# Optimization experiments

Hardware: AMD Instinct MI355X
Metric: run time of the kernel (lower is better)

The kernel has to match this reference:

```python
import jax, jax.numpy as jnp
import numpy as np

BN_EPS = 1e-5
ELU_ALPHA = 512.0  # bug-faithful: nn.ELU(in_channels) sets alpha=in_channels


def conv3x3(x, w):
    # NCHW input, OIHW kernel, stride 1, padding 1 (SAME for k=3)
    return jax.lax.conv_general_dilated(
        x, w, window_strides=(1, 1), padding=((1, 1), (1, 1)),
        dimension_numbers=('NCHW', 'OIHW', 'NCHW'))


def conv1x1(x, w, b):
    # 1x1 conv as a channel contraction
    return jnp.einsum('oc,bchw->bohw', w[:, :, 0, 0], x) + b[None, :, None, None]


def batchnorm(x, g, b, m, v):
    scale = g / jnp.sqrt(v + BN_EPS)
    return (x - m[None, :, None, None]) * scale[None, :, None, None] + b[None, :, None, None]


def cc_module(x, wq, bq, wk, bk, wv, bv, gamma):
    B, C, H, W = x.shape
    q = conv1x1(x, wq, bq)   # [B, C/8, H, W]
    k = conv1x1(x, wk, bk)   # [B, C/8, H, W]
    v = conv1x1(x, wv, bv)   # [B, C,   H, W]
    # column (H-axis) attention scores with -inf on the self-diagonal
    eH = jnp.einsum('bchw,bcgw->bhwg', q, k)              # [B,H,W,H]
    diag = jnp.eye(H, dtype=bool)[None, :, None, :]       # mask h == g
    eH = jnp.where(diag, -jnp.inf, eH)
    # row (W-axis) attention scores
    eW = jnp.einsum('bchw,bchv->bhwv', q, k)              # [B,H,W,W]
    att = jax.nn.softmax(jnp.concatenate([eH, eW], axis=-1), axis=-1)  # [B,H,W,H+W]
    aH, aW = att[..., :H], att[..., H:]
    oH = jnp.einsum('bcgw,bhwg->bchw', v, aH)
    oW = jnp.einsum('bchv,bhwv->bchw', v, aW)
    return gamma[0] * (oH + oW) + x


def setup_inputs() -> dict:
    key = jax.random.key(0)
    ks = jax.random.split(key, 20)
    B, Cin, H, W = 8, 512, 64, 64
    Ci = Cin // 4            # 128
    Cq = Ci // 8             # 16
    n = lambda k, s, sc: jax.random.normal(k, s, dtype=jnp.float32) * sc
    inp = {
        'x': n(ks[0], (B, Cin, H, W), 1.0),
        'conva_w': n(ks[1], (Ci, Cin, 3, 3), 0.02),
        'bn1_g': jax.random.uniform(ks[2], (Ci,)) + 0.5,
        'bn1_b': n(ks[3], (Ci,), 0.1),
        'bn1_m': n(ks[4], (Ci,), 0.1),
        'bn1_v': jax.random.uniform(ks[5], (Ci,)) + 0.5,
        'wq': n(ks[6], (Cq, Ci, 1, 1), 0.05),
        'bq': n(ks[7], (Cq,), 0.02),
        'wk': n(ks[8], (Cq, Ci, 1, 1), 0.05),
        'bk': n(ks[9], (Cq,), 0.02),
        'wv': n(ks[10], (Ci, Ci, 1, 1), 0.05),
        'bv': n(ks[11], (Ci,), 0.02),
        'cc_gamma': jnp.full((1,), 0.5, dtype=jnp.float32),
        'convb_w': n(ks[12], (Ci, Ci, 3, 3), 0.05),
        'bn2_g': jax.random.uniform(ks[13], (Ci,)) + 0.5,
        'bn2_b': n(ks[14], (Ci,), 0.1),
        'bn2_m': n(ks[15], (Ci,), 0.1),
        'bn2_v': jax.random.uniform(ks[16], (Ci,)) + 0.5,
        'bott_w': n(ks[17], (Cin, Cin + Ci, 3, 3), 0.02),
        'recurrence': 2,
    }
    return inp


def reference(x, conva_w, bn1_g, bn1_b, bn1_m, bn1_v,
              wq, bq, wk, bk, wv, bv, cc_gamma,
              convb_w, bn2_g, bn2_b, bn2_m, bn2_v,
              bott_w, recurrence):
    out = batchnorm(conv3x3(x, conva_w), bn1_g, bn1_b, bn1_m, bn1_v)
    for _ in range(int(recurrence)):
        out = cc_module(out, wq, bq, wk, bk, wv, bv, cc_gamma)
    out = batchnorm(conv3x3(out, convb_w), bn2_g, bn2_b, bn2_m, bn2_v)
    out = conv3x3(jnp.concatenate([x, out], axis=1), bott_w)
    # ELU with alpha = in_channels (faithful to nn.ELU(in_channels))
    return jnp.where(out > 0, out, ELU_ALPHA * jnp.expm1(out))
```

## Files before the change

### kernel.cpp

```cpp
#include <hip/hip_runtime.h>
#include <math.h>


typedef __attribute__((ext_vector_type(8))) short short8;
typedef __attribute__((ext_vector_type(4))) float f32x4;

__device__ __forceinline__ unsigned short f2bf(float x) {
    unsigned u = __float_as_uint(x);
    unsigned r = u + 0x7FFFu + ((u >> 16) & 1u);
    return (unsigned short)(r >> 16);
}
__device__ __forceinline__ float bf2f(unsigned short h) {
    return __uint_as_float(((unsigned)h) << 16);
}

__global__ __launch_bounds__(256) void prep_bn_kernel(
        const float* g1, const float* b1, const float* m1, const float* v1,
        const float* g2, const float* b2, const float* m2, const float* v2,
        float* s1o, float* h1o, float* s2o, float* h2o) {
    int t = threadIdx.x;
    if (t < 128) {
        float s = g1[t] * __frsqrt_rn(v1[t] + 1e-5f);
        s1o[t] = s; h1o[t] = b1[t] - m1[t] * s;
    } else {
        int c = t - 128;
        float s = g2[c] * __frsqrt_rn(v2[c] + 1e-5f);
        s2o[c] = s; h2o[c] = b2[c] - m2[c] * s;
    }
}

__global__ __launch_bounds__(256) void prep_w_kernel(
        const float* __restrict__ w, unsigned short* __restrict__ WH,
        unsigned short* __restrict__ WL, int CIN, int COUT) {
    int idx = blockIdx.x * 256 + threadIdx.x;
    if (idx >= COUT * CIN) return;
    int cout = idx / CIN, ci = idx - cout * CIN;
    #pragma unroll
    for (int tap = 0; tap < 9; ++tap) {
        float v = w[(size_t)idx * 9 + tap];
        unsigned short h = f2bf(v);
        unsigned short l = f2bf(v - bf2f(h));
        size_t o = ((size_t)tap * COUT + cout) * CIN + ci;
        WH[o] = h; WL[o] = l;
    }
}

__global__ __launch_bounds__(256) void prep_qkv_kernel(
        const float* __restrict__ wq, const float* __restrict__ wk,
        const float* __restrict__ wv,
        float* __restrict__ wqk_t, float* __restrict__ wv_t) {
    int e = blockIdx.x * 256 + threadIdx.x;
    if (e < 4096) {
        int ci = e >> 5, co = e & 31;
        wqk_t[e] = (co < 16) ? wq[co * 128 + ci] : wk[(co - 16) * 128 + ci];
    } else if (e < 4096 + 16384) {
        int e2 = e - 4096;
        int ci = e2 >> 7, co = e2 & 127;
        wv_t[e2] = wv[co * 128 + ci];
    }
}

__global__ __launch_bounds__(256) void transpose_cl_kernel(
        const float* __restrict__ in, float* __restrict__ out, int NCH) {
    __shared__ float T[32][260];
    const int t = threadIdx.x;
    const int h0 = blockIdx.x * 4, b = blockIdx.y, ck = blockIdx.z;
    const float* base = in + (size_t)(b * NCH + ck) * 32 * 4096;
    const int ci = t >> 3, w0 = (t & 7) * 8;
    #pragma unroll
    for (int hh = 0; hh < 4; ++hh) {
        float4 u0 = *(const float4*)&base[(size_t)ci * 4096 + (h0 + hh) * 64 + w0];
        float4 u1 = *(const float4*)&base[(size_t)ci * 4096 + (h0 + hh) * 64 + w0 + 4];
        T[ci][hh * 65 + w0 + 0] = u0.x; T[ci][hh * 65 + w0 + 1] = u0.y;
        T[ci][hh * 65 + w0 + 2] = u0.z; T[ci][hh * 65 + w0 + 3] = u0.w;
        T[ci][hh * 65 + w0 + 4] = u1.x; T[ci][hh * 65 + w0 + 5] = u1.y;
        T[ci][hh * 65 + w0 + 6] = u1.z; T[ci][hh * 65 + w0 + 7] = u1.w;
    }
    __syncthreads();
    const int w = t & 63, hh2 = t >> 6;
    float* op = out + ((size_t)((b * NCH + ck) * 4096) + (h0 + hh2) * 64 + w) * 32;
    #pragma unroll
    for (int cg = 0; cg < 8; ++cg) {
        float4 r;
        r.x = T[cg * 4 + 0][hh2 * 65 + w];
        r.y = T[cg * 4 + 1][hh2 * 65 + w];
        r.z = T[cg * 4 + 2][hh2 * 65 + w];
        r.w = T[cg * 4 + 3][hh2 * 65 + w];
        *(float4*)&op[cg * 4] = r;
    }
}

template<int NCHUNK, int COUT, int EPI, int C1CH>
__global__ __launch_bounds__(256, 2) void conv3x3_mfma_kernel(
        const float* __restrict__ xt1, const float* __restrict__ xt2,
        const unsigned short* __restrict__ WH, const unsigned short* __restrict__ WL,
        const float* __restrict__ bns, const float* __restrict__ bnb,
        float* __restrict__ out) {
    constexpr int CINF = NCHUNK * 32;
    __shared__ unsigned short XS[2][4][66][40];
    __shared__ unsigned short WAs[2][64][104];
    const int t = threadIdx.x;
    const int lane = t & 63, wave = t >> 6;
    const int ch = wave >> 1, o = wave & 1;
    const int ln = lane & 15, lg = lane >> 4;
    const int h0 = blockIdx.x * 2, b = blockIdx.y, cb0 = blockIdx.z * 64;

    if (t < 32) {
        int r = t >> 3, s = (t >> 2) & 1, cig = t & 3;
        short8 z = {};
        *(short8*)&XS[0][r][s * 65][cig * 8] = z;
        *(short8*)&XS[1][r][s * 65][cig * 8] = z;
    }

    f32x4 acc[2][4];
    #pragma unroll
    for (int mi = 0; mi < 2; ++mi)
        #pragma unroll
        for (int q = 0; q < 4; ++q) acc[mi][q] = (f32x4){0.f, 0.f, 0.f, 0.f};

    const int xr = t >> 6, xw = t & 63;
    for (int chunk = 0; chunk < NCHUNK; ++chunk) {
        const float* src = (chunk < C1CH)
            ? xt1 + (size_t)(b * C1CH + chunk) * 4096 * 32
            : xt2 + (size_t)(b * (NCHUNK - C1CH) + (chunk - C1CH)) * 4096 * 32;
        {
            int row = h0 - 1 + xr;
            if (row >= 0 && row < 64) {
                const float* sp = src + ((size_t)row * 64 + xw) * 32;
                #pragma unroll
                for (int cg = 0; cg < 4; ++cg) {
                    float4 u0 = *(const float4*)&sp[cg * 8];
                    float4 u1 = *(const float4*)&sp[cg * 8 + 4];
                    float xv[8] = {u0.x, u0.y, u0.z, u0.w, u1.x, u1.y, u1.z, u1.w};
                    short8 hi, lo;
                    #pragma unroll
                    for (int j = 0; j < 8; ++j) {
                        unsigned short hb = f2bf(xv[j]);
                        hi[j] = (short)hb;
                        lo[j] = (short)f2bf(xv[j] - bf2f(hb));
                    }
                    *(short8*)&XS[0][xr][1 + xw][cg * 8] = hi;
                    *(short8*)&XS[1][xr][1 + xw][cg * 8] = lo;
                }
            } else {
                short8 z = {};
                #pragma unroll
                for (int cg = 0; cg < 4; ++cg) {
                    *(short8*)&XS[0][xr][1 + xw][cg * 8] = z;
                    *(short8*)&XS[1][xr][1 + xw][cg * 8] = z;
                }
            }
        }
        const int ci0 = chunk * 32;
        for (int kh = 0; kh < 3; ++kh) {
            #pragma unroll
            for (int i = 0; i < 3; ++i) {
                int e = t + i * 256;
                int cout = e / 12, r2 = e - cout * 12;
                int kw = r2 >> 2, cig = r2 & 3;
                size_t go = ((size_t)(kh * 3 + kw) * COUT + cb0 + cout) * CINF + ci0 + cig * 8;
                *(short8*)&WAs[0][cout][kw * 32 + cig * 8] = *(const short8*)&WH[go];
                *(short8*)&WAs[1][cout][kw * 32 + cig * 8] = *(const short8*)&WL[go];
            }
            __syncthreads();
            const int row = o + kh;
            #pragma unroll
            for (int kw = 0; kw < 3; ++kw) {
                short8 ah0 = *(const short8*)&WAs[0][ch * 32 + ln][kw * 32 + lg * 8];
                short8 ah1 = *(const short8*)&WAs[0][ch * 32 + 16 + ln][kw * 32 + lg * 8];
                short8 al0 = *(const short8*)&WAs[1][ch * 32 + ln][kw * 32 + lg * 8];
                short8 al1 = *(const short8*)&WAs[1][ch * 32 + 16 + ln][kw * 32 + lg * 8];
                #pragma unroll
                for (int q = 0; q < 4; ++q) {
                    short8 bh = *(const short8*)&XS[0][row][q * 16 + ln + kw][lg * 8];
                    short8 bl = *(const short8*)&XS[1][row][q * 16 + ln + kw][lg * 8];
                    acc[0][q] = __builtin_amdgcn_mfma_f32_16x16x32_bf16(ah0, bh, acc[0][q], 0, 0, 0);
                    acc[1][q] = __builtin_amdgcn_mfma_f32_16x16x32_bf16(ah1, bh, acc[1][q], 0, 0, 0);
                    acc[0][q] = __builtin_amdgcn_mfma_f32_16x16x32_bf16(ah0, bl, acc[0][q], 0, 0, 0);
                    acc[1][q] = __builtin_amdgcn_mfma_f32_16x16x32_bf16(ah1, bl, acc[1][q], 0, 0, 0);
                    acc[0][q] = __builtin_amdgcn_mfma_f32_16x16x32_bf16(al0, bh, acc[0][q], 0, 0, 0);
                    acc[1][q] = __builtin_amdgcn_mfma_f32_16x16x32_bf16(al1, bh, acc[1][q], 0, 0, 0);
                }
            }
            __syncthreads();
        }
    }
    const int hh = h0 + o;
    #pragma unroll
    for (int mi = 0; mi < 2; ++mi) {
        #pragma unroll
        for (int q = 0; q < 4; ++q) {
            #pragma unroll
            for (int reg = 0; reg < 4; ++reg) {
                int cout = cb0 + ch * 32 + mi * 16 + lg * 4 + reg;
                int wv2 = q * 16 + ln;
                float val = acc[mi][q][reg];
                if (EPI == 0) val = val * bns[cout] + bnb[cout];
                else          val = (val > 0.f) ? val : 512.0f * expm1f(val);
                out[((size_t)(b * COUT + cout) * 64 + hh) * 64 + wv2] = val;
            }
        }
    }
}

__global__ __launch_bounds__(256) void qk_kernel(
        const float* __restrict__ X, const float* __restrict__ wqk_t,
        const float* __restrict__ bq, const float* __restrict__ bk,
        float* __restrict__ q, float* __restrict__ k) {
    __shared__ float xls[128][64];
    __shared__ float wls[128][32];
    const int t = threadIdx.x;
    const int h = blockIdx.x, b = blockIdx.y;
    const float* xb = X + (size_t)b * 128 * 4096 + (size_t)h * 64;
    #pragma unroll
    for (int i = 0; i < 32; ++i) {
        int e = t + i * 256;
        xls[e >> 6][e & 63] = xb[(size_t)(e >> 6) * 4096 + (e & 63)];
    }
    #pragma unroll
    for (int i = 0; i < 16; ++i) {
        int e = t + i * 256;
        wls[e >> 5][e & 31] = wqk_t[e];
    }
    __syncthreads();
    const int w = t & 63, g = t >> 6;
    const int co0 = g * 8;
    float acc[8];
    #pragma unroll
    for (int c = 0; c < 8; ++c) acc[c] = 0.f;
    #pragma unroll 8
    for (int ci = 0; ci < 128; ++ci) {
        float xv = xls[ci][w];
        float4 wa = *(const float4*)&wls[ci][co0];
        float4 wb = *(const float4*)&wls[ci][co0 + 4];
        const float* pa = (const float*)&wa;
        const float* pb = (const float*)&wb;
        #pragma unroll
        for (int c = 0; c < 4; ++c) { acc[c] += pa[c] * xv; acc[4 + c] += pb[c] * xv; }
    }
    #pragma unroll
    for (int c = 0; c < 8; ++c) {
        int co = co0 + c;
        if (co < 16) q[((size_t)(b * 16 + co) * 64 + h) * 64 + w]      = acc[c] + bq[co];
        else         k[((size_t)(b * 16 + co - 16) * 64 + h) * 64 + w] = acc[c] + bk[co - 16];
    }
}

__global__ __launch_bounds__(256) void v_kernel(
        const float* __restrict__ X, const float* __restrict__ wv_t,
        const float* __restrict__ bv, float* __restrict__ v) {
    __shared__ float xls[16][64];
    __shared__ float wls[16][128];
    const int t = threadIdx.x;
    const int n0 = blockIdx.x * 64, b = blockIdx.y;
    const int wt = t & 15, ct = t >> 4;
    const float* xb = X + (size_t)b * 128 * 4096;
    float acc[8][4] = {};
    for (int ci0 = 0; ci0 < 128; ci0 += 16) {
        #pragma unroll
        for (int i = 0; i < 4; ++i) {
            int e = t + i * 256;
            xls[e >> 6][e & 63] = xb[(size_t)(ci0 + (e >> 6)) * 4096 + n0 + (e & 63)];
        }
        #pragma unroll
        for (int i = 0; i < 8; ++i) {
            int e = t + i * 256;
            wls[e >> 7][e & 127] = wv_t[(size_t)(ci0 + (e >> 7)) * 128 + (e & 127)];
        }
        __syncthreads();
        #pragma unroll 4
        for (int ci = 0; ci < 16; ++ci) {
            float4 xv = *(const float4*)&xls[ci][wt * 4];
            float4 wa = *(const float4*)&wls[ci][ct * 8];
            float4 wb = *(const float4*)&wls[ci][ct * 8 + 4];
            const float* px = (const float*)&xv;
            const float* pa = (const float*)&wa;
            const float* pb = (const float*)&wb;
            #pragma unroll
            for (int j = 0; j < 4; ++j)
                #pragma unroll
                for (int c = 0; c < 4; ++c) {
                    acc[c][j]     += pa[c] * px[j];
                    acc[4 + c][j] += pb[c] * px[j];
                }
        }
        __syncthreads();
    }
    #pragma unroll
    for (int c = 0; c < 8; ++c) {
        int co = ct * 8 + c;
        float bb = bv[co];
        float4 r = {acc[c][0] + bb, acc[c][1] + bb, acc[c][2] + bb, acc[c][3] + bb};
        *(float4*)&v[(size_t)(b * 128 + co) * 4096 + n0 + wt * 4] = r;
    }
}

__global__ __launch_bounds__(256) void eh_kernel(
        const float* __restrict__ q, const float* __restrict__ k,
        float* __restrict__ att) {
    __shared__ float qs[16][64];
    __shared__ float ks[16][64];
    const int t = threadIdx.x;
    const int w = blockIdx.x, b = blockIdx.y;
    #pragma unroll
    for (int i = 0; i < 4; ++i) {
        int e = t + i * 256;
        int c = e >> 6, h = e & 63;
        size_t idx = ((size_t)(b * 16 + c) * 64 + h) * 64 + w;
        qs[c][h] = q[idx];
        ks[c][h] = k[idx];
    }
    __syncthreads();
    const int g0 = (t & 15) * 4, h0 = (t >> 4) * 4;
    float acc[4][4] = {};
    #pragma unroll
    for (int c = 0; c < 16; ++c) {
        float4 qv = *(const float4*)&qs[c][h0];
        float4 kv = *(const float4*)&ks[c][g0];
        const float* pq = (const float*)&qv;
        const float* pk = (const float*)&kv;
        #pragma unroll
        for (int i = 0; i < 4; ++i)
            #pragma unroll
            for (int j = 0; j < 4; ++j) acc[i][j] += pq[i] * pk[j];
    }
    #pragma unroll
    for (int i = 0; i < 4; ++i) {
        int h = h0 + i;
        int dj = h - g0;
        if (dj >= 0 && dj < 4) acc[i][dj] = -1e30f;
        float4 r = {acc[i][0], acc[i][1], acc[i][2], acc[i][3]};
        *(float4*)&att[((size_t)(b * 64 + h) * 64 + w) * 128 + g0] = r;
    }
}

__global__ __launch_bounds__(256) void ew_kernel(
        const float* __restrict__ q, const float* __restrict__ k,
        float* __restrict__ att) {
    __shared__ float qs[16][64];
    __shared__ float ks[16][64];
    const int t = threadIdx.x;
    const int h = blockIdx.x, b = blockIdx.y;
    const float* qb2 = q + (size_t)b * 65536 + (size_t)h * 64;
    const float* kb2 = k + (size_t)b * 65536 + (size_t)h * 64;
    #pragma unroll
    for (int i = 0; i < 4; ++i) {
        int e = t + i * 256;
        int c = e >> 6, wl = e & 63;
        qs[c][wl] = qb2[(size_t)c * 4096 + wl];
        ks[c][wl] = kb2[(size_t)c * 4096 + wl];
    }
    __syncthreads();
    const int tt0 = (t & 15) * 4, w0 = (t >> 4) * 4;
    float acc[4][4] = {};
    #pragma unroll
    for (int c = 0; c < 16; ++c) {
        float4 qv = *(const float4*)&qs[c][w0];
        float4 kv = *(const float4*)&ks[c][tt0];
        const float* pq = (const float*)&qv;
        const float* pk = (const float*)&kv;
        #pragma unroll
        for (int i = 0; i < 4; ++i)
            #pragma unroll
            for (int j = 0; j < 4; ++j) acc[i][j] += pq[i] * pk[j];
    }
    #pragma unroll
    for (int i = 0; i < 4; ++i) {
        float4 r = {acc[i][0], acc[i][1], acc[i][2], acc[i][3]};
        *(float4*)&att[((size_t)(b * 64 + h) * 64 + (w0 + i)) * 128 + 64 + tt0] = r;
    }
}

__global__ __launch_bounds__(128) void softmax_kernel(float* __restrict__ att) {
    const int r = blockIdx.x, t = threadIdx.x;
    float v = att[(size_t)r * 128 + t];
    float m = v;
    #pragma unroll
    for (int off = 32; off >= 1; off >>= 1) m = fmaxf(m, __shfl_xor(m, off));
    __shared__ float s1[2], s2[2];
    const int wid = t >> 6, lane = t & 63;
    if (lane == 0) s1[wid] = m;
    __syncthreads();
    m = fmaxf(s1[0], s1[1]);
    float e = expf(v - m);
    float s = e;
    #pragma unroll
    for (int off = 32; off >= 1; off >>= 1) s += __shfl_xor(s, off);
    if (lane == 0) s2[wid] = s;
    __syncthreads();
    s = s2[0] + s2[1];
    att[(size_t)r * 128 + t] = e / s;
}

__global__ __launch_bounds__(256) void oh_kernel(
        const float* __restrict__ v, const float* __restrict__ att,
        float* __restrict__ ohb) {
    __shared__ float vs2[64][128];
    __shared__ float ah2[64][65];
    const int t = threadIdx.x;
    const int w = blockIdx.x, b = blockIdx.y;
    const float* vbp = v + (size_t)b * 524288 + w;
    #pragma unroll
    for (int i = 0; i < 32; ++i) {
        int e = t + i * 256;
        vs2[e >> 7][e & 127] = vbp[((size_t)(e & 127) * 64 + (e >> 7)) * 64];
    }
    const float* abp = att + ((size_t)b * 4096 + w) * 128;
    #pragma unroll
    for (int i = 0; i < 16; ++i) {
        int e = t + i * 256;
        ah2[e >> 6][e & 63] = abp[(size_t)(e >> 6) * 8192 + (e & 63)];
    }
    __syncthreads();
    const int h0 = (t & 15) * 4, c0 = (t >> 4) * 8;
    float acc[8][4] = {};
    for (int g = 0; g < 64; ++g) {
        float4 va  = *(const float4*)&vs2[g][c0];
        float4 vb4 = *(const float4*)&vs2[g][c0 + 4];
        const float* pa = (const float*)&va;
        const float* pb = (const float*)&vb4;
        float aj[4];
        #pragma unroll
        for (int j = 0; j < 4; ++j) aj[j] = ah2[h0 + j][g];
        #pragma unroll
        for (int j = 0; j < 4; ++j)
            #pragma unroll
            for (int i2 = 0; i2 < 4; ++i2) {
                acc[i2][j]     += pa[i2] * aj[j];
                acc[4 + i2][j] += pb[i2] * aj[j];
            }
    }
    #pragma unroll
    for (int i2 = 0; i2 < 8; ++i2)
        #pragma unroll
        for (int j = 0; j < 4; ++j)
            ohb[((size_t)(b * 128 + c0 + i2) * 64 + (h0 + j)) * 64 + w] = acc[i2][j];
}

__global__ __launch_bounds__(256) void ow_final_kernel(
        const float* __restrict__ v, const float* __restrict__ att,
        const float* __restrict__ ohb, const float* __restrict__ gamma,
        const float* __restrict__ Xin, float* __restrict__ Xout) {
    __shared__ float vs2[64][129];
    __shared__ float aws[64][65];
    const int t = threadIdx.x;
    const int h = blockIdx.x, b = blockIdx.y;
    const float* vbp = v + (size_t)b * 524288 + (size_t)h * 64;
    #pragma unroll
    for (int i = 0; i < 32; ++i) {
        int e = t + i * 256;
        vs2[e & 63][e >> 6] = vbp[(size_t)(e >> 6) * 4096 + (e & 63)];
    }
    const float* abp = att + ((size_t)(b * 64 + h) * 64) * 128 + 64;
    #pragma unroll
    for (int i = 0; i < 16; ++i) {
        int e = t + i * 256;
        aws[e >> 6][e & 63] = abp[(size_t)(e >> 6) * 128 + (e & 63)];
    }
    __syncthreads();
    const int w0 = (t & 15) * 4, c0 = (t >> 4) * 8;
    float acc[8][4] = {};
    for (int tt = 0; tt < 64; ++tt) {
        float vv[8];
        #pragma unroll
        for (int i2 = 0; i2 < 8; ++i2) vv[i2] = vs2[tt][c0 + i2];
        float aw[4];
        #pragma unroll
        for (int j = 0; j < 4; ++j) aw[j] = aws[w0 + j][tt];
        #pragma unroll
        for (int i2 = 0; i2 < 8; ++i2)
            #pragma unroll
            for (int j = 0; j < 4; ++j) acc[i2][j] += vv[i2] * aw[j];
    }
    const float gm = gamma[0];
    #pragma unroll
    for (int i2 = 0; i2 < 8; ++i2) {
        size_t base = ((size_t)(b * 128 + c0 + i2) * 64 + h) * 64 + w0;
        float4 oh4 = *(const float4*)&ohb[base];
        float4 xr  = *(const float4*)&Xin[base];
        const float* po = (const float*)&oh4;
        const float* px = (const float*)&xr;
        float4 r;
        float* pr = (float*)&r;
        #pragma unroll
        for (int j = 0; j < 4; ++j) pr[j] = gm * (acc[i2][j] + po[j]) + px[j];
        *(float4*)&Xout[base] = r;
    }
}

extern "C" void kernel_launch(void* const* d_in, const int* in_sizes, int n_in,
                              void* d_out, int out_size, void* d_ws, size_t ws_size,
                              hipStream_t stream) {
    const float* x       = (const float*)d_in[0];
    const float* conva_w = (const float*)d_in[1];
    const float* bn1_g   = (const float*)d_in[2];
    const float* bn1_b   = (const float*)d_in[3];
    const float* bn1_m   = (const float*)d_in[4];
    const float* bn1_v   = (const float*)d_in[5];
    const float* wq      = (const float*)d_in[6];
    const float* bq      = (const float*)d_in[7];
    const float* wk      = (const float*)d_in[8];
    const float* bk      = (const float*)d_in[9];
    const float* wv      = (const float*)d_in[10];
    const float* bv      = (const float*)d_in[11];
    const float* gamma   = (const float*)d_in[12];
    const float* convb_w = (const float*)d_in[13];
    const float* bn2_g   = (const float*)d_in[14];
    const float* bn2_b   = (const float*)d_in[15];
    const float* bn2_m   = (const float*)d_in[16];
    const float* bn2_v   = (const float*)d_in[17];
    const float* bott_w  = (const float*)d_in[18];

    float* ws    = (float*)d_ws;
    float* A     = ws;
    float* Bb    = A     + 4194304;
    float* vbuf  = Bb    + 4194304;
    float* attb  = vbuf  + 4194304;
    float* ohb   = attb  + 4194304;
    float* qb    = ohb   + 4194304;
    float* kb    = qb    + 524288;
    float* XT_x  = kb    + 524288;
    float* wqk_t = XT_x  + 16777216;
    float* wv_t  = wqk_t + 4096;
    float* bnsA  = wv_t  + 16384;
    float* bnbA  = bnsA  + 128;
    float* bnsB  = bnbA  + 128;
    float* bnbB  = bnsB  + 128;
    unsigned short* WHa = (unsigned short*)(bnbB + 128);
    unsigned short* WLa = WHa + 589824;
    unsigned short* WHb = WLa + 589824;
    unsigned short* WLb = WHb + 147456;
    unsigned short* WHc = WLb + 147456;
    unsigned short* WLc = WHc + 2949120;
    float* XT_cc = vbuf;
    float* XT_b  = attb;

    prep_bn_kernel<<<1, 256, 0, stream>>>(bn1_g, bn1_b, bn1_m, bn1_v,
                                          bn2_g, bn2_b, bn2_m, bn2_v,
                                          bnsA, bnbA, bnsB, bnbB);
    prep_w_kernel<<<256, 256, 0, stream>>>(conva_w, WHa, WLa, 512, 128);
    prep_w_kernel<<<64, 256, 0, stream>>>(convb_w, WHb, WLb, 128, 128);
    prep_w_kernel<<<1280, 256, 0, stream>>>(bott_w, WHc, WLc, 640, 512);
    prep_qkv_kernel<<<80, 256, 0, stream>>>(wq, wk, wv, wqk_t, wv_t);

    transpose_cl_kernel<<<dim3(16, 8, 16), 256, 0, stream>>>(x, XT_x, 16);

    conv3x3_mfma_kernel<16, 128, 0, 16><<<dim3(32, 8, 2), 256, 0, stream>>>(
        XT_x, nullptr, WHa, WLa, bnsA, bnbA, A);

    float* Xi = A;
    float* Xo = Bb;
    for (int it = 0; it < 2; ++it) {
        qk_kernel<<<dim3(64, 8), 256, 0, stream>>>(Xi, wqk_t, bq, bk, qb, kb);
        v_kernel<<<dim3(64, 8), 256, 0, stream>>>(Xi, wv_t, bv, vbuf);
        eh_kernel<<<dim3(64, 8), 256, 0, stream>>>(qb, kb, attb);
        ew_kernel<<<dim3(64, 8), 256, 0, stream>>>(qb, kb, attb);
        softmax_kernel<<<32768, 128, 0, stream>>>(attb);
        oh_kernel<<<dim3(64, 8), 256, 0, stream>>>(vbuf, attb, ohb);
        ow_final_kernel<<<dim3(64, 8), 256, 0, stream>>>(vbuf, attb, ohb, gamma, Xi, Xo);
        float* tmp = Xi; Xi = Xo; Xo = tmp;
    }

    transpose_cl_kernel<<<dim3(16, 8, 4), 256, 0, stream>>>(Xi, XT_cc, 4);
    conv3x3_mfma_kernel<4, 128, 0, 4><<<dim3(32, 8, 2), 256, 0, stream>>>(
        XT_cc, nullptr, WHb, WLb, bnsB, bnbB, Bb);

    transpose_cl_kernel<<<dim3(16, 8, 4), 256, 0, stream>>>(Bb, XT_b, 4);
    conv3x3_mfma_kernel<20, 512, 1, 16><<<dim3(32, 8, 8), 256, 0, stream>>>(
        XT_x, XT_b, WHc, WLc, nullptr, nullptr, (float*)d_out);
}
```

Baseline: 1.223 ms.

## Rewrite conv3x3 with presplit bf16 inputs, 32x32 MFMA, async LDS loads; fuse softmax

The transpose kernel now splits activations into hi/lo bf16 planes in padded, halo-aware layout, so the conv kernel no longer converts fp32 on the fly. The conv kernel is restructured to use 32x32x16 bf16 MFMA with 128-thread blocks covering 4 output rows and half the width. It loads inputs via global_load_lds directly into shared memory and streams weights from a repacked per-chunk layout straight into registers with one-tap prefetch. Separately, the ew-score and softmax kernels are fused to avoid an extra pass over the attention buffer. The changes trade a larger workspace and register pressure from 8 16-wide accumulators for less conversion and launch overhead.

```diff
diff --git a/kernel.cpp b/kernel.cpp
--- a/kernel.cpp
+++ b/kernel.cpp
@@ -2,8 +2,9 @@
 #include <math.h>
 
 
-typedef __attribute__((ext_vector_type(8))) short short8;
-typedef __attribute__((ext_vector_type(4))) float f32x4;
+typedef __attribute__((ext_vector_type(8)))  short short8;
+typedef __attribute__((ext_vector_type(4)))  float f32x4;
+typedef __attribute__((ext_vector_type(16))) float f32x16;
 
 __device__ __forceinline__ unsigned short f2bf(float x) {
     unsigned u = __float_as_uint(x);
@@ -12,6 +13,20 @@
 }
 __device__ __forceinline__ float bf2f(unsigned short h) {
     return __uint_as_float(((unsigned)h) << 16);
+}
+__device__ __forceinline__ void split2(float a, float b, unsigned& hi, unsigned& lo) {
+    unsigned h;
+    asm("v_cvt_pk_bf16_f32 %0, %1, %2" : "=v"(h) : "v"(a), "v"(b));
+    float ra = a - __uint_as_float(h << 16);
+    float rb = b - __uint_as_float(h & 0xffff0000u);
+    unsigned l;
+    asm("v_cvt_pk_bf16_f32 %0, %1, %2" : "=v"(l) : "v"(ra), "v"(rb));
+    hi = h; lo = l;
+}
+__device__ __forceinline__ void gll16(const unsigned short* g, unsigned short* l) {
+    __builtin_amdgcn_global_load_lds(
+        (const __attribute__((address_space(1))) unsigned int*)g,
+        (__attribute__((address_space(3))) unsigned int*)l, 16, 0, 0);
 }
 
 __global__ __launch_bounds__(256) void prep_bn_kernel(
@@ -29,19 +44,20 @@
     }
 }
 
-__global__ __launch_bounds__(256) void prep_w_kernel(
-        const float* __restrict__ w, unsigned short* __restrict__ WH,
-        unsigned short* __restrict__ WL, int CIN, int COUT) {
+__global__ __launch_bounds__(256) void prep_w2(
+        const float* __restrict__ w, unsigned short* __restrict__ Wp, int CIN, int COUT) {
     int idx = blockIdx.x * 256 + threadIdx.x;
     if (idx >= COUT * CIN) return;
     int cout = idx / CIN, ci = idx - cout * CIN;
+    int ck = ci >> 5, cl = ci & 31;
     #pragma unroll
     for (int tap = 0; tap < 9; ++tap) {
         float v = w[(size_t)idx * 9 + tap];
         unsigned short h = f2bf(v);
         unsigned short l = f2bf(v - bf2f(h));
-        size_t o = ((size_t)tap * COUT + cout) * CIN + ci;
-        WH[o] = h; WL[o] = l;
+        size_t rb = (((size_t)ck * 9 + tap) * 2 * COUT + cout) * 32;
+        Wp[rb + cl] = h;
+        Wp[rb + (size_t)COUT * 32 + cl] = l;
     }
 }
 
@@ -60,8 +76,8 @@
     }
 }
 
-__global__ __launch_bounds__(256) void transpose_cl_kernel(
-        const float* __restrict__ in, float* __restrict__ out, int NCH) {
+__global__ __launch_bounds__(256) void transpose_split_kernel(
+        const float* __restrict__ in, unsigned short* __restrict__ out, int NCH) {
     __shared__ float T[32][260];
     const int t = threadIdx.x;
     const int h0 = blockIdx.x * 4, b = blockIdx.y, ck = blockIdx.z;
@@ -78,126 +94,155 @@
     }
     __syncthreads();
     const int w = t & 63, hh2 = t >> 6;
-    float* op = out + ((size_t)((b * NCH + ck) * 4096) + (h0 + hh2) * 64 + w) * 32;
-    #pragma unroll
-    for (int cg = 0; cg < 8; ++cg) {
-        float4 r;
-        r.x = T[cg * 4 + 0][hh2 * 65 + w];
-        r.y = T[cg * 4 + 1][hh2 * 65 + w];
-        r.z = T[cg * 4 + 2][hh2 * 65 + w];
-        r.w = T[cg * 4 + 3][hh2 * 65 + w];
-        *(float4*)&op[cg * 4] = r;
+    const int h = h0 + hh2;
+    const size_t PL = (size_t)64 * 68 * 40;
+    unsigned short* po = out + ((size_t)(b * NCH + ck) * 2) * PL;
+    unsigned hi[16], lo[16];
+    #pragma unroll
+    for (int p = 0; p < 16; ++p) {
+        float a = T[2 * p][hh2 * 65 + w];
+        float c = T[2 * p + 1][hh2 * 65 + w];
+        split2(a, c, hi[p], lo[p]);
+    }
+    uint4 zz = {0u, 0u, 0u, 0u};
+    #pragma unroll
+    for (int half = 0; half < 2; ++half) {
+        bool ok = half ? (w >= 31) : (w <= 32);
+        int slot = half ? (w - 31) : (w + 1);
+        if (ok) {
+            unsigned short* ph = po + ((size_t)h * 68 + half * 34 + slot) * 40;
+            unsigned short* pl = ph + PL;
+            #pragma unroll
+            for (int q = 0; q < 4; ++q) {
+                uint4 hv = {hi[q * 4], hi[q * 4 + 1], hi[q * 4 + 2], hi[q * 4 + 3]};
+                uint4 lv = {lo[q * 4], lo[q * 4 + 1], lo[q * 4 + 2], lo[q * 4 + 3]};
+                *(uint4*)(ph + q * 8) = hv;
+                *(uint4*)(pl + q * 8) = lv;
+            }
+            *(uint4*)(ph + 32) = zz;
+            *(uint4*)(pl + 32) = zz;
+        }
+    }
+    if (w == 0 || w == 63) {
+        int half = (w == 63);
+        int slot = half ? 33 : 0;
+        unsigned short* ph = po + ((size_t)h * 68 + half * 34 + slot) * 40;
+        #pragma unroll
+        for (int q = 0; q < 5; ++q) {
+            *(uint4*)(ph + q * 8) = zz;
+            *(uint4*)(ph + PL + q * 8) = zz;
+        }
     }
 }
 
 template<int NCHUNK, int COUT, int EPI, int C1CH>
-__global__ __launch_bounds__(256, 2) void conv3x3_mfma_kernel(
-        const float* __restrict__ xt1, const float* __restrict__ xt2,
-        const unsigned short* __restrict__ WH, const unsigned short* __restrict__ WL,
+__global__ __launch_bounds__(128, 2) void conv3x3_g(
+        const unsigned short* __restrict__ xt1, const unsigned short* __restrict__ xt2,
+        const unsigned short* __restrict__ Wp,
         const float* __restrict__ bns, const float* __restrict__ bnb,
         float* __restrict__ out) {
-    constexpr int CINF = NCHUNK * 32;
-    __shared__ unsigned short XS[2][4][66][40];
-    __shared__ unsigned short WAs[2][64][104];
-    const int t = threadIdx.x;
-    const int lane = t & 63, wave = t >> 6;
-    const int ch = wave >> 1, o = wave & 1;
-    const int ln = lane & 15, lg = lane >> 4;
-    const int h0 = blockIdx.x * 2, b = blockIdx.y, cb0 = blockIdx.z * 64;
-
-    if (t < 32) {
-        int r = t >> 3, s = (t >> 2) & 1, cig = t & 3;
-        short8 z = {};
-        *(short8*)&XS[0][r][s * 65][cig * 8] = z;
-        *(short8*)&XS[1][r][s * 65][cig * 8] = z;
-    }
-
-    f32x4 acc[2][4];
-    #pragma unroll
-    for (int mi = 0; mi < 2; ++mi)
-        #pragma unroll
-        for (int q = 0; q < 4; ++q) acc[mi][q] = (f32x4){0.f, 0.f, 0.f, 0.f};
-
-    const int xr = t >> 6, xw = t & 63;
+    __shared__ __align__(16) unsigned short XS[2][6][34][40];
+    const int t = threadIdx.x;
+    const int lane = t & 63, ch = t >> 6;
+    const int lw = lane & 31, kg = lane >> 5;
+    const int h0 = blockIdx.x * 4;
+    const int b  = blockIdx.y;
+    const int cz = blockIdx.z >> 1, wz = blockIdx.z & 1;
+    const int cb0 = cz * 128;
+    const size_t XPLANE = (size_t)64 * 68 * 40;
+    constexpr int HLSTR = 6 * 34 * 40;
+
+    const f32x16 fz = {0.f,0.f,0.f,0.f,0.f,0.f,0.f,0.f,0.f,0.f,0.f,0.f,0.f,0.f,0.f,0.f};
+    f32x16 acc[2][4];
+    #pragma unroll
+    for (int mt = 0; mt < 2; ++mt)
+        #pragma unroll
+        for (int r = 0; r < 4; ++r) acc[mt][r] = fz;
+
+    #pragma unroll 1
     for (int chunk = 0; chunk < NCHUNK; ++chunk) {
-        const float* src = (chunk < C1CH)
-            ? xt1 + (size_t)(b * C1CH + chunk) * 4096 * 32
-            : xt2 + (size_t)(b * (NCHUNK - C1CH) + (chunk - C1CH)) * 4096 * 32;
-        {
-            int row = h0 - 1 + xr;
-            if (row >= 0 && row < 64) {
-                const float* sp = src + ((size_t)row * 64 + xw) * 32;
-                #pragma unroll
-                for (int cg = 0; cg < 4; ++cg) {
-                    float4 u0 = *(const float4*)&sp[cg * 8];
-                    float4 u1 = *(const float4*)&sp[cg * 8 + 4];
-                    float xv[8] = {u0.x, u0.y, u0.z, u0.w, u1.x, u1.y, u1.z, u1.w};
-                    short8 hi, lo;
-                    #pragma unroll
-                    for (int j = 0; j < 8; ++j) {
-                        unsigned short hb = f2bf(xv[j]);
-                        hi[j] = (short)hb;
-                        lo[j] = (short)f2bf(xv[j] - bf2f(hb));
-                    }
-                    *(short8*)&XS[0][xr][1 + xw][cg * 8] = hi;
-                    *(short8*)&XS[1][xr][1 + xw][cg * 8] = lo;
-                }
+        const unsigned short* xb = (chunk < C1CH)
+            ? xt1 + ((size_t)(b * C1CH + chunk) * 2) * XPLANE
+            : xt2 + ((size_t)(b * (NCHUNK - C1CH) + (chunk - C1CH)) * 2) * XPLANE;
+        #pragma unroll
+        for (int j = 0; j < 6; ++j) {
+            const int grow = h0 - 1 + j;
+            unsigned short* ld = &XS[ch][j][0][0];
+            if (grow >= 0 && grow < 64) {
+                const unsigned short* g = xb + (size_t)ch * XPLANE + ((size_t)grow * 68 + wz * 34) * 40;
+                gll16(g + (size_t)lane * 8, ld + (size_t)lane * 8);
+                gll16(g + (size_t)(64 + lane) * 8, ld + (size_t)(64 + lane) * 8);
+                if (lane < 42)
+                    gll16(g + (size_t)(128 + lane) * 8, ld + (size_t)(128 + lane) * 8);
             } else {
                 short8 z = {};
+                *(short8*)(ld + (size_t)lane * 8) = z;
+                *(short8*)(ld + (size_t)(64 + lane) * 8) = z;
+                if (lane < 42) *(short8*)(ld + (size_t)(128 + lane) * 8) = z;
+            }
+        }
+        __syncthreads();
+
+        const unsigned short* wbase = Wp + (size_t)chunk * (9 * 2 * (size_t)COUT * 32);
+        const int crow = cb0 + ch * 64 + lw;
+        short8 wc[8], wn[8];
+        {
+            const unsigned short* ph = wbase + ((size_t)0 * COUT + crow) * 32 + kg * 8;
+            const unsigned short* pl = ph + (size_t)COUT * 32;
+            wc[0] = *(const short8*)(ph);             wc[1] = *(const short8*)(ph + 32 * 32);
+            wc[2] = *(const short8*)(pl);             wc[3] = *(const short8*)(pl + 32 * 32);
+            wc[4] = *(const short8*)(ph + 16);        wc[5] = *(const short8*)(ph + 32 * 32 + 16);
+            wc[6] = *(const short8*)(pl + 16);        wc[7] = *(const short8*)(pl + 32 * 32 + 16);
+        }
+        #pragma unroll 1
+        for (int tap = 0; tap < 9; ++tap) {
+            {
+                const int tn = (tap < 8) ? tap + 1 : 0;
+                const unsigned short* ph = wbase + ((size_t)(tn * 2) * COUT + crow) * 32 + kg * 8;
+                const unsigned short* pl = ph + (size_t)COUT * 32;
+                wn[0] = *(const short8*)(ph);         wn[1] = *(const short8*)(ph + 32 * 32);
+                wn[2] = *(const short8*)(pl);         wn[3] = *(const short8*)(pl + 32 * 32);
+                wn[4] = *(const short8*)(ph + 16);    wn[5] = *(const short8*)(ph + 32 * 32 + 16);
+                wn[6] = *(const short8*)(pl + 16);    wn[7] = *(const short8*)(pl + 32 * 32 + 16);
+            }
+            const int kh = (tap < 3) ? 0 : ((tap < 6) ? 1 : 2);
+            const int kw = tap - kh * 3;
+            #pragma unroll
+            for (int ks = 0; ks < 2; ++ks) {
+                const short8 ah0 = wc[ks * 4 + 0], ah1 = wc[ks * 4 + 1];
+                const short8 al0 = wc[ks * 4 + 2], al1 = wc[ks * 4 + 3];
+                const int ko = ks * 16 + kg * 8;
                 #pragma unroll
-                for (int cg = 0; cg < 4; ++cg) {
-                    *(short8*)&XS[0][xr][1 + xw][cg * 8] = z;
-                    *(short8*)&XS[1][xr][1 + xw][cg * 8] = z;
+                for (int r = 0; r < 4; ++r) {
+                    const unsigned short* xp = &XS[0][r + kh][lw + kw][ko];
+                    short8 bh = *(const short8*)xp;
+                    short8 bl = *(const short8*)(xp + HLSTR);
+                    acc[0][r] = __builtin_amdgcn_mfma_f32_32x32x16_bf16(ah0, bh, acc[0][r], 0, 0, 0);
+                    acc[1][r] = __builtin_amdgcn_mfma_f32_32x32x16_bf16(ah1, bh, acc[1][r], 0, 0, 0);
+                    acc[0][r] = __builtin_amdgcn_mfma_f32_32x32x16_bf16(ah0, bl, acc[0][r], 0, 0, 0);
+                    acc[1][r] = __builtin_amdgcn_mfma_f32_32x32x16_bf16(ah1, bl, acc[1][r], 0, 0, 0);
+                    acc[0][r] = __builtin_amdgcn_mfma_f32_32x32x16_bf16(al0, bh, acc[0][r], 0, 0, 0);
+                    acc[1][r] = __builtin_amdgcn_mfma_f32_32x32x16_bf16(al1, bh, acc[1][r], 0, 0, 0);
                 }
             }
-        }
-        const int ci0 = chunk * 32;
-        for (int kh = 0; kh < 3; ++kh) {
-            #pragma unroll
-            for (int i = 0; i < 3; ++i) {
-                int e = t + i * 256;
-                int cout = e / 12, r2 = e - cout * 12;
-                int kw = r2 >> 2, cig = r2 & 3;
-                size_t go = ((size_t)(kh * 3 + kw) * COUT + cb0 + cout) * CINF + ci0 + cig * 8;
-                *(short8*)&WAs[0][cout][kw * 32 + cig * 8] = *(const short8*)&WH[go];
-                *(short8*)&WAs[1][cout][kw * 32 + cig * 8] = *(const short8*)&WL[go];
-            }
-            __syncthreads();
-            const int row = o + kh;
-            #pragma unroll
-            for (int kw = 0; kw < 3; ++kw) {
-                short8 ah0 = *(const short8*)&WAs[0][ch * 32 + ln][kw * 32 + lg * 8];
-                short8 ah1 = *(const short8*)&WAs[0][ch * 32 + 16 + ln][kw * 32 + lg * 8];
-                short8 al0 = *(const short8*)&WAs[1][ch * 32 + ln][kw * 32 + lg * 8];
-                short8 al1 = *(const short8*)&WAs[1][ch * 32 + 16 + ln][kw * 32 + lg * 8];
-                #pragma unroll
-                for (int q = 0; q < 4; ++q) {
-                    short8 bh = *(const short8*)&XS[0][row][q * 16 + ln + kw][lg * 8];
-                    short8 bl = *(const short8*)&XS[1][row][q * 16 + ln + kw][lg * 8];
-                    acc[0][q] = __builtin_amdgcn_mfma_f32_16x16x32_bf16(ah0, bh, acc[0][q], 0, 0, 0);
-                    acc[1][q] = __builtin_amdgcn_mfma_f32_16x16x32_bf16(ah1, bh, acc[1][q], 0, 0, 0);
-                    acc[0][q] = __builtin_amdgcn_mfma_f32_16x16x32_bf16(ah0, bl, acc[0][q], 0, 0, 0);
-                    acc[1][q] = __builtin_amdgcn_mfma_f32_16x16x32_bf16(ah1, bl, acc[1][q], 0, 0, 0);
-                    acc[0][q] = __builtin_amdgcn_mfma_f32_16x16x32_bf16(al0, bh, acc[0][q], 0, 0, 0);
-                    acc[1][q] = __builtin_amdgcn_mfma_f32_16x16x32_bf16(al1, bh, acc[1][q], 0, 0, 0);
-                }
-            }
-            __syncthreads();
-        }
-    }
-    const int hh = h0 + o;
-    #pragma unroll
-    for (int mi = 0; mi < 2; ++mi) {
-        #pragma unroll
-        for (int q = 0; q < 4; ++q) {
-            #pragma unroll
-            for (int reg = 0; reg < 4; ++reg) {
-                int cout = cb0 + ch * 32 + mi * 16 + lg * 4 + reg;
-                int wv2 = q * 16 + ln;
-                float val = acc[mi][q][reg];
+            #pragma unroll
+            for (int i = 0; i < 8; ++i) wc[i] = wn[i];
+        }
+        __syncthreads();
+    }
+    #pragma unroll
+    for (int mt = 0; mt < 2; ++mt) {
+        #pragma unroll
+        for (int r = 0; r < 4; ++r) {
+            const int orow = h0 + r;
+            #pragma unroll
+            for (int reg = 0; reg < 16; ++reg) {
+                const int m = (reg & 3) + 8 * (reg >> 2) + 4 * kg;
+                const int cout = cb0 + ch * 64 + mt * 32 + m;
+                float val = acc[mt][r][reg];
                 if (EPI == 0) val = val * bns[cout] + bnb[cout];
                 else          val = (val > 0.f) ? val : 512.0f * expm1f(val);
-                out[((size_t)(b * COUT + cout) * 64 + hh) * 64 + wv2] = val;
+                out[((size_t)(b * COUT + cout) * 64 + orow) * 64 + wz * 32 + lw] = val;
             }
         }
     }
@@ -334,11 +379,14 @@
     }
 }
 
-__global__ __launch_bounds__(256) void ew_kernel(
+__global__ __launch_bounds__(256) void ew_softmax_kernel(
         const float* __restrict__ q, const float* __restrict__ k,
         float* __restrict__ att) {
     __shared__ float qs[16][64];
     __shared__ float ks[16][64];
+    __shared__ float ehs[64][65];
+    __shared__ float ews[64][65];
+    __shared__ float sinv[64];
     const int t = threadIdx.x;
     const int h = blockIdx.x, b = blockIdx.y;
     const float* qb2 = q + (size_t)b * 65536 + (size_t)h * 64;
@@ -349,6 +397,12 @@
         int c = e >> 6, wl = e & 63;
         qs[c][wl] = qb2[(size_t)c * 4096 + wl];
         ks[c][wl] = kb2[(size_t)c * 4096 + wl];
+    }
+    float* abase = att + (size_t)(b * 64 + h) * 64 * 128;
+    #pragma unroll
+    for (int i = 0; i < 16; ++i) {
+        int e = t + i * 256;
+        ehs[e >> 6][e & 63] = abase[(size_t)(e >> 6) * 128 + (e & 63)];
     }
     __syncthreads();
     const int tt0 = (t & 15) * 4, w0 = (t >> 4) * 4;
@@ -365,31 +419,35 @@
             for (int j = 0; j < 4; ++j) acc[i][j] += pq[i] * pk[j];
     }
     #pragma unroll
-    for (int i = 0; i < 4; ++i) {
-        float4 r = {acc[i][0], acc[i][1], acc[i][2], acc[i][3]};
-        *(float4*)&att[((size_t)(b * 64 + h) * 64 + (w0 + i)) * 128 + 64 + tt0] = r;
-    }
-}
-
-__global__ __launch_bounds__(128) void softmax_kernel(float* __restrict__ att) {
-    const int r = blockIdx.x, t = threadIdx.x;
-    float v = att[(size_t)r * 128 + t];
-    float m = v;
-    #pragma unroll
-    for (int off = 32; off >= 1; off >>= 1) m = fmaxf(m, __shfl_xor(m, off));
-    __shared__ float s1[2], s2[2];
-    const int wid = t >> 6, lane = t & 63;
-    if (lane == 0) s1[wid] = m;
-    __syncthreads();
-    m = fmaxf(s1[0], s1[1]);
-    float e = expf(v - m);
-    float s = e;
-    #pragma unroll
-    for (int off = 32; off >= 1; off >>= 1) s += __shfl_xor(s, off);
-    if (lane == 0) s2[wid] = s;
-    __syncthreads();
-    s = s2[0] + s2[1];
-    att[(size_t)r * 128 + t] = e / s;
+    for (int i = 0; i < 4; ++i)
+        #pragma unroll
+        for (int j = 0; j < 4; ++j) ews[w0 + i][tt0 + j] = acc[i][j];
+    __syncthreads();
+    const int r = t >> 2, qd = t & 3;
+    float* src = (qd < 2) ? &ehs[r][qd * 32] : &ews[r][(qd - 2) * 32];
+    float m = -3.0e38f;
+    #pragma unroll
+    for (int kk = 0; kk < 32; ++kk) m = fmaxf(m, src[kk]);
+    m = fmaxf(m, __shfl_xor(m, 1));
+    m = fmaxf(m, __shfl_xor(m, 2));
+    float s = 0.f;
+    #pragma unroll
+    for (int kk = 0; kk < 32; ++kk) {
+        float e = expf(src[kk] - m);
+        src[kk] = e;
+        s += e;
+    }
+    s += __shfl_xor(s, 1);
+    s += __shfl_xor(s, 2);
+    if (qd == 0) sinv[r] = 1.0f / s;
+    __syncthreads();
+    #pragma unroll
+    for (int i = 0; i < 32; ++i) {
+        int e = t + i * 256;
+        int row = e >> 7, col = e & 127;
+        float vsm = (col < 64) ? ehs[row][col] : ews[row][col - 64];
+        abase[(size_t)row * 128 + col] = vsm * sinv[row];
+    }
 }
 
 __global__ __launch_bounds__(256) void oh_kernel(
@@ -511,42 +569,40 @@
     const float* bn2_v   = (const float*)d_in[17];
     const float* bott_w  = (const float*)d_in[18];
 
-    float* ws    = (float*)d_ws;
-    float* A     = ws;
-    float* Bb    = A     + 4194304;
-    float* vbuf  = Bb    + 4194304;
-    float* attb  = vbuf  + 4194304;
-    float* ohb   = attb  + 4194304;
-    float* qb    = ohb   + 4194304;
-    float* kb    = qb    + 524288;
-    float* XT_x  = kb    + 524288;
-    float* wqk_t = XT_x  + 16777216;
+    float* ws   = (float*)d_ws;
+    float* A    = ws;
+    float* Bb   = A    + 4194304;
+    float* vbuf = Bb   + 4194304;
+    float* attb = vbuf + 4194304;
+    float* ohb  = attb + 4194304;
+    float* qb   = ohb  + 4194304;
+    float* kb   = qb   + 524288;
+    unsigned short* XT_x = (unsigned short*)(kb + 524288);
+    float* after_xt = kb + 524288 + 22282240;
+    unsigned short* Wp_a = (unsigned short*)after_xt;
+    unsigned short* Wp_b = Wp_a + 1179648;
+    unsigned short* Wp_c = Wp_b + 294912;
+    float* wqk_t = (float*)(Wp_c + 5898240);
     float* wv_t  = wqk_t + 4096;
-    float* bnsA  = wv_t  + 16384;
-    float* bnbA  = bnsA  + 128;
-    float* bnsB  = bnbA  + 128;
-    float* bnbB  = bnsB  + 128;
-    unsigned short* WHa = (unsigned short*)(bnbB + 128);
-    unsigned short* WLa = WHa + 589824;
-    unsigned short* WHb = WLa + 589824;
-    unsigned short* WLb = WHb + 147456;
-    unsigned short* WHc = WLb + 147456;
-    unsigned short* WLc = WHc + 2949120;
-    float* XT_cc = vbuf;
-    float* XT_b  = attb;
+    float* bnsA  = wv_t + 16384;
+    float* bnbA  = bnsA + 128;
+    float* bnsB  = bnbA + 128;
+    float* bnbB  = bnsB + 128;
+    unsigned short* XT_cc = (unsigned short*)vbuf;
+    unsigned short* XT_b  = XT_cc + 11141120;
 
     prep_bn_kernel<<<1, 256, 0, stream>>>(bn1_g, bn1_b, bn1_m, bn1_v,
                                           bn2_g, bn2_b, bn2_m, bn2_v,
                                           bnsA, bnbA, bnsB, bnbB);
-    prep_w_kernel<<<256, 256, 0, stream>>>(conva_w, WHa, WLa, 512, 128);
-    prep_w_kernel<<<64, 256, 0, stream>>>(convb_w, WHb, WLb, 128, 128);
-    prep_w_kernel<<<1280, 256, 0, stream>>>(bott_w, WHc, WLc, 640, 512);
+    prep_w2<<<256, 256, 0, stream>>>(conva_w, Wp_a, 512, 128);
+    prep_w2<<<64, 256, 0, stream>>>(convb_w, Wp_b, 128, 128);
+    prep_w2<<<1280, 256, 0, stream>>>(bott_w, Wp_c, 640, 512);
     prep_qkv_kernel<<<80, 256, 0, stream>>>(wq, wk, wv, wqk_t, wv_t);
 
-    transpose_cl_kernel<<<dim3(16, 8, 16), 256, 0, stream>>>(x, XT_x, 16);
-
-    conv3x3_mfma_kernel<16, 128, 0, 16><<<dim3(32, 8, 2), 256, 0, stream>>>(
-        XT_x, nullptr, WHa, WLa, bnsA, bnbA, A);
+    transpose_split_kernel<<<dim3(16, 8, 16), 256, 0, stream>>>(x, XT_x, 16);
+
+    conv3x3_g<16, 128, 0, 16><<<dim3(16, 8, 2), 128, 0, stream>>>(
+        XT_x, nullptr, Wp_a, bnsA, bnbA, A);
 
     float* Xi = A;
     float* Xo = Bb;
@@ -554,18 +610,17 @@
         qk_kernel<<<dim3(64, 8), 256, 0, stream>>>(Xi, wqk_t, bq, bk, qb, kb);
         v_kernel<<<dim3(64, 8), 256, 0, stream>>>(Xi, wv_t, bv, vbuf);
         eh_kernel<<<dim3(64, 8), 256, 0, stream>>>(qb, kb, attb);
-        ew_kernel<<<dim3(64, 8), 256, 0, stream>>>(qb, kb, attb);
-        softmax_kernel<<<32768, 128, 0, stream>>>(attb);
+        ew_softmax_kernel<<<dim3(64, 8), 256, 0, stream>>>(qb, kb, attb);
         oh_kernel<<<dim3(64, 8), 256, 0, stream>>>(vbuf, attb, ohb);
         ow_final_kernel<<<dim3(64, 8), 256, 0, stream>>>(vbuf, attb, ohb, gamma, Xi, Xo);
         float* tmp = Xi; Xi = Xo; Xo = tmp;
     }
 
-    transpose_cl_kernel<<<dim3(16, 8, 4), 256, 0, stream>>>(Xi, XT_cc, 4);
-    conv3x3_mfma_kernel<4, 128, 0, 4><<<dim3(32, 8, 2), 256, 0, stream>>>(
-        XT_cc, nullptr, WHb, WLb, bnsB, bnbB, Bb);
-
-    transpose_cl_kernel<<<dim3(16, 8, 4), 256, 0, stream>>>(Bb, XT_b, 4);
-    conv3x3_mfma_kernel<20, 512, 1, 16><<<dim3(32, 8, 8), 256, 0, stream>>>(
-        XT_x, XT_b, WHc, WLc, nullptr, nullptr, (float*)d_out);
-}
+    transpose_split_kernel<<<dim3(16, 8, 4), 256, 0, stream>>>(Xi, XT_cc, 4);
+    conv3x3_g<4, 128, 0, 4><<<dim3(16, 8, 2), 128, 0, stream>>>(
+        XT_cc, nullptr, Wp_b, bnsB, bnbB, Bb);
+
+    transpose_split_kernel<<<dim3(16, 8, 4), 256, 0, stream>>>(Bb, XT_b, 4);
+    conv3x3_g<20, 512, 1, 16><<<dim3(16, 8, 8), 128, 0, stream>>>(
+        XT_x, XT_b, Wp_c, nullptr, nullptr, (float*)d_out);
+}
```

Result: no change. 1.227 ms (+0.3%).
